# Kernel tuning notes

Measured on AMD Instinct MI355X. Metric: run time of the kernel, lower is better.

Reference implementation:

```python
import jax, jax.numpy as jnp
import numpy as np

B, S, HID, H, DH = 8, 4096, 1024, 16, 64


def setup_inputs() -> dict:
    key = jax.random.key(0)
    ks = jax.random.split(key, 5)
    return {
        "hidden_states": jax.random.normal(ks[0], (B, S, HID), dtype=jnp.float32),
        "attention_mask": jnp.ones((B, 1, 1, S), dtype=jnp.float32),
        "Wq": jax.random.normal(ks[1], (HID, HID), dtype=jnp.float32) * (HID ** -0.5),
        "Wk": jax.random.normal(ks[2], (HID, HID), dtype=jnp.float32) * (HID ** -0.5),
        "Wv": jax.random.normal(ks[3], (HID, HID), dtype=jnp.float32) * (HID ** -0.5),
        "att_weight": jax.random.normal(ks[4], (H, 1, DH), dtype=jnp.float32) * (DH ** -0.5),
    }


def _heads(x):
    # [B,S,HID] -> [B,H,S,DH]
    b, s, _ = x.shape
    return x.reshape(b, s, H, DH).transpose(0, 2, 1, 3)


def reference(hidden_states, attention_mask, Wq, Wk, Wv, att_weight):
    # bias-free projections (torch Linear: x @ W.T)
    q = _heads(hidden_states @ Wq.T)  # [B,H,S,DH]
    k = _heads(hidden_states @ Wk.T)
    v = _heads(hidden_states @ Wv.T)

    mask = attention_mask.transpose(0, 1, 3, 2)  # [B,1,S,1]
    aw = att_weight[:, 0, :]  # [H,DH]

    q_scores = jnp.einsum('bhsd,hd->bhs', q, aw)[..., None] * mask  # [B,H,S,1]
    k_scores = jnp.einsum('bhsd,hd->bhs', k, aw)[..., None] * mask  # [B,H,S,1]

    length = jnp.sum(mask, axis=-2, keepdims=True)            # [B,1,1,1]
    mean_value = jnp.sum(v * mask, axis=-2, keepdims=True)    # [B,H,1,DH]

    query_values = q_scores * mean_value                      # [B,H,S,DH] outer product
    key_values = jnp.einsum('bhs,bhsd->bhd', k_scores[..., 0], v)[:, :, None, :]  # [B,H,1,DH]

    ctx = (query_values + key_values) / length                # [B,H,S,DH]
    ctx = ctx.transpose(0, 2, 1, 3).reshape(ctx.shape[0], ctx.shape[2], H * DH)
    return ctx
```

## Files before the change

### kernel.cpp

```cpp
#include <hip/hip_runtime.h>

#define BB 8
#define SS 4096
#define HIDD 1024
#define HH 16
#define DHH 64

__global__ __launch_bounds__(256) void k_prep(const float* __restrict__ Wq,
                                              const float* __restrict__ Wk,
                                              const float* __restrict__ aw,
                                              float* __restrict__ wq_f,
                                              float* __restrict__ wk_f) {
    int i = blockIdx.x * 256 + threadIdx.x;
    int h = blockIdx.y;
    const float* W = blockIdx.z ? Wk : Wq;
    float* outp = blockIdx.z ? wk_f : wq_f;
    float acc = 0.f;
#pragma unroll
    for (int d = 0; d < DHH; ++d) {
        acc += aw[h * DHH + d] * W[(size_t)(h * DHH + d) * HIDD + i];
    }
    outp[h * HIDD + i] = acc;
}

#define KC 64
#define NCH (HIDD / KC)
__global__ __launch_bounds__(512) void k_scores(const float* __restrict__ hid,
                                                const float* __restrict__ mask,
                                                const float* __restrict__ weff,
                                                float* __restrict__ qsb,
                                                float* __restrict__ ksb) {
    __shared__ float shh[2][128 * 17 * 4];
    __shared__ float shw[2][32 * 16 * 4];

    const int t    = threadIdx.x;
    const int lane = t & 63;
    const int wave = t >> 6;
    const int obase = __builtin_amdgcn_readfirstlane(wave * 4);

    const int row0 = blockIdx.x * 128 + lane;
    const int row1 = row0 + 64;
    const size_t gbase = (size_t)blockIdx.x * 128 * HIDD;

    int srow[5], scol[5];
#pragma unroll
    for (int j = 0; j < 5; ++j) {
        int f = (j < 4) ? (j * 512 + t) : (2048 + t);
        int r = f / 17;
        int c = f - r * 17;
        srow[j] = r;
        scol[j] = (c == 16) ? 0 : c;
    }
    const bool extra = (t < 128);

    auto stage = [&](int chunk, int buf) {
#pragma unroll
        for (int j = 0; j < 4; ++j) {
            const float* gp = hid + gbase + (size_t)srow[j] * HIDD
                              + chunk * KC + scol[j] * 4;
            float* lp = &shh[buf][(j * 512 + t) * 4];
            __builtin_amdgcn_global_load_lds(
                (const __attribute__((address_space(1))) void*)gp,
                (__attribute__((address_space(3))) void*)lp, 16, 0, 0);
        }
        if (extra) {
            const float* gp = hid + gbase + (size_t)srow[4] * HIDD
                              + chunk * KC + scol[4] * 4;
            float* lp = &shh[buf][(2048 + t) * 4];
            __builtin_amdgcn_global_load_lds(
                (const __attribute__((address_space(1))) void*)gp,
                (__attribute__((address_space(3))) void*)lp, 16, 0, 0);
        }
        {
            const float* gp = weff + (size_t)(t >> 4) * HIDD
                              + chunk * KC + (t & 15) * 4;
            float* lp = &shw[buf][t * 4];
            __builtin_amdgcn_global_load_lds(
                (const __attribute__((address_space(1))) void*)gp,
                (__attribute__((address_space(3))) void*)lp, 16, 0, 0);
        }
    };

    float acc0[4] = {0.f, 0.f, 0.f, 0.f};
    float acc1[4] = {0.f, 0.f, 0.f, 0.f};

    stage(0, 0);

    for (int chunk = 0; chunk < NCH; ++chunk) {
        const int buf = chunk & 1;
        asm volatile("s_waitcnt vmcnt(0)" ::: "memory");
        __syncthreads();
        if (chunk + 1 < NCH) stage(chunk + 1, buf ^ 1);

        const float* h0 = &shh[buf][lane * 68];
        const float* h1 = &shh[buf][(lane + 64) * 68];
        const float* wb = &shw[buf][obase * 64];
#pragma unroll
        for (int kc = 0; kc < 16; ++kc) {
            float4 a0 = *reinterpret_cast<const float4*>(h0 + kc * 4);
            float4 a1 = *reinterpret_cast<const float4*>(h1 + kc * 4);
#pragma unroll
            for (int o = 0; o < 4; ++o) {
                float4 wv = *reinterpret_cast<const float4*>(wb + o * 64 + kc * 4);
                acc0[o] += a0.x * wv.x + a0.y * wv.y + a0.z * wv.z + a0.w * wv.w;
                acc1[o] += a1.x * wv.x + a1.y * wv.y + a1.z * wv.z + a1.w * wv.w;
            }
        }
    }

    float m0 = mask[row0];
    float m1 = mask[row1];
#pragma unroll
    for (int o = 0; o < 4; ++o) { acc0[o] *= m0; acc1[o] *= m1; }

    float4 v0 = make_float4(acc0[0], acc0[1], acc0[2], acc0[3]);
    float4 v1 = make_float4(acc1[0], acc1[1], acc1[2], acc1[3]);
    if (obase < 16) {
        *reinterpret_cast<float4*>(qsb + (size_t)row0 * 16 + obase) = v0;
        *reinterpret_cast<float4*>(qsb + (size_t)row1 * 16 + obase) = v1;
    } else {
        *reinterpret_cast<float4*>(ksb + (size_t)row0 * 20 + (obase - 16)) = v0;
        *reinterpret_cast<float4*>(ksb + (size_t)row1 * 20 + (obase - 16)) = v1;
        if (obase == 16) {
            ksb[(size_t)row0 * 20 + 16] = m0;
            ksb[(size_t)row1 * 20 + 16] = m1;
        }
    }
}

__global__ __launch_bounds__(256) void k_ksh(const float* __restrict__ hid,
                                             const float* __restrict__ ksb,
                                             float* __restrict__ part) {
    int b  = blockIdx.y;
    int i  = threadIdx.x * 4;
    int s0 = blockIdx.x * 64;

    float4 acc[17];
#pragma unroll
    for (int c = 0; c < 17; ++c) acc[c] = make_float4(0.f, 0.f, 0.f, 0.f);

    const float* hb = hid + (size_t)(b * SS + s0) * HIDD + i;
    const float* sb = ksb + (size_t)(b * SS + s0) * 20;

#pragma unroll 4
    for (int s = 0; s < 64; ++s) {
        float4 hv = *reinterpret_cast<const float4*>(hb + (size_t)s * HIDD);
        const float* sc = sb + s * 20;
#pragma unroll
        for (int c = 0; c < 17; ++c) {
            float scv = sc[c];
            acc[c].x += scv * hv.x;
            acc[c].y += scv * hv.y;
            acc[c].z += scv * hv.z;
            acc[c].w += scv * hv.w;
        }
    }

    float* pb = part + (((size_t)blockIdx.x * 8 + b) * 17) * 1024 + i;
#pragma unroll
    for (int c = 0; c < 17; ++c) {
        *reinterpret_cast<float4*>(pb + c * 1024) = acc[c];
    }
}

__global__ __launch_bounds__(256) void k_red(const float* __restrict__ part,
                                             float* __restrict__ ksh,
                                             float* __restrict__ hsum) {
    int gid = blockIdx.x * 256 + threadIdx.x;
    int b = gid / 17408;
    int r = gid - b * 17408;
    int c = r >> 10;
    int i = r & 1023;

    float s = 0.f;
#pragma unroll 8
    for (int k = 0; k < 64; ++k)
        s += part[(((size_t)k * 8 + b) * 17 + c) * 1024 + i];

    if (c < 16) ksh[((size_t)b * 16 + c) * 1024 + i] = s;
    else        hsum[b * 1024 + i] = s;
}

__global__ __launch_bounds__(256) void k_fin(const float* __restrict__ Wv,
                                             const float* __restrict__ mask,
                                             const float* __restrict__ hsum,
                                             const float* __restrict__ ksh,
                                             float* __restrict__ mvn,
                                             float* __restrict__ kvn) {
    int b  = blockIdx.x;
    int j  = blockIdx.y * 32 + (threadIdx.x >> 3);
    int sl = threadIdx.x & 7;

    __shared__ float red[256];
    float lsum = 0.f;
    for (int s = threadIdx.x; s < SS; s += 256) lsum += mask[b * SS + s];
    red[threadIdx.x] = lsum;
    __syncthreads();
    for (int off = 128; off; off >>= 1) {
        if (threadIdx.x < off) red[threadIdx.x] += red[threadIdx.x + off];
        __syncthreads();
    }
    float invlen = 1.0f / red[0];

    int h = j >> 6;
    const float4* w4 = reinterpret_cast<const float4*>(Wv + (size_t)j * HIDD + sl * 128);
    const float4* hv = reinterpret_cast<const float4*>(hsum + b * HIDD + sl * 128);
    const float4* kv = reinterpret_cast<const float4*>(ksh + ((size_t)b * 16 + h) * HIDD + sl * 128);

    float mv = 0.f, kvv = 0.f;
#pragma unroll
    for (int c = 0; c < 32; ++c) {
        float4 w = w4[c], a = hv[c], k2 = kv[c];
        mv  += w.x * a.x  + w.y * a.y  + w.z * a.z  + w.w * a.w;
        kvv += w.x * k2.x + w.y * k2.y + w.z * k2.z + w.w * k2.w;
    }
#pragma unroll
    for (int off = 1; off < 8; off <<= 1) {
        mv  += __shfl_xor(mv, off);
        kvv += __shfl_xor(kvv, off);
    }
    if (sl == 0) {
        mvn[b * HIDD + j] = mv * invlen;
        kvn[b * HIDD + j] = kvv * invlen;
    }
}

__global__ __launch_bounds__(256) void k_out(const float* __restrict__ qsb,
                                             const float* __restrict__ mvn,
                                             const float* __restrict__ kvn,
                                             float* __restrict__ outp) {
    size_t e0 = ((size_t)blockIdx.x * 256 + threadIdx.x) * 8;
    int b   = (int)(e0 >> 22);
    int rem = (int)(e0 & ((1u << 22) - 1));
    int s   = rem >> 10;
    int j   = rem & 1023;

    float q = qsb[(size_t)(b * SS + s) * 16 + (j >> 6)];
    const float4* mv4 = reinterpret_cast<const float4*>(mvn + b * HIDD + j);
    const float4* kv4 = reinterpret_cast<const float4*>(kvn + b * HIDD + j);
    float4 m0 = mv4[0], m1 = mv4[1];
    float4 k0 = kv4[0], k1 = kv4[1];

    float4 o0, o1;
    o0.x = q * m0.x + k0.x;  o0.y = q * m0.y + k0.y;
    o0.z = q * m0.z + k0.z;  o0.w = q * m0.w + k0.w;
    o1.x = q * m1.x + k1.x;  o1.y = q * m1.y + k1.y;
    o1.z = q * m1.z + k1.z;  o1.w = q * m1.w + k1.w;

    float4* op = reinterpret_cast<float4*>(outp + e0);
    op[0] = o0;
    op[1] = o1;
}

extern "C" void kernel_launch(void* const* d_in, const int* in_sizes, int n_in,
                              void* d_out, int out_size, void* d_ws, size_t ws_size,
                              hipStream_t stream) {
    const float* hid  = (const float*)d_in[0];
    const float* mask = (const float*)d_in[1];
    const float* Wq   = (const float*)d_in[2];
    const float* Wk   = (const float*)d_in[3];
    const float* Wv   = (const float*)d_in[4];
    const float* aw   = (const float*)d_in[5];
    float* outp = (float*)d_out;

    float* ws   = (float*)d_ws;
    float* wq_f = ws;
    float* wk_f = wq_f + 16384;
    float* qsb  = wk_f + 16384;
    float* ksb  = qsb + 524288;
    float* ksh  = ksb + 655360;
    float* hsum = ksh + 131072;
    float* mvn  = hsum + 8192;
    float* kvn  = mvn + 8192;
    float* part = kvn + 8192;

    k_prep  <<<dim3(4, 16, 2), 256, 0, stream>>>(Wq, Wk, aw, wq_f, wk_f);
    k_scores<<<dim3(256),      512, 0, stream>>>(hid, mask, wq_f, qsb, ksb);
    k_ksh   <<<dim3(64, 8),    256, 0, stream>>>(hid, ksb, part);
    k_red   <<<dim3(544),      256, 0, stream>>>(part, ksh, hsum);
    k_fin   <<<dim3(8, 32),    256, 0, stream>>>(Wv, mask, hsum, ksh, mvn, kvn);
    k_out   <<<dim3(16384),    256, 0, stream>>>(qsb, mvn, kvn, outp);
}
```

Before: 346.2 us.

## Compute score projections with split-bf16 MFMA instead of FP32 FMA

The k_scores GEMM (hidden x 32 effective weight columns) now runs on bf16 MFMA 16x16x32 instructions. Each fp32 value is split into hi+lo bf16 parts and three products are summed to stay close to fp32 accuracy. k_prep now writes the weights pre-split and pre-packed in the MFMA B-operand layout. The tile shrinks to 64 rows per 256-thread block with twice as many blocks. This cuts the FP32 ALU cost of the score GEMM, at the price of per-element conversion work on the A operand and some accuracy risk from the 3-term split.

```diff
diff --git a/kernel.cpp b/kernel.cpp
--- a/kernel.cpp
+++ b/kernel.cpp
@@ -6,59 +6,75 @@
 #define HH 16
 #define DHH 64
 
+typedef __attribute__((ext_vector_type(8))) short bf16x8;
+typedef __attribute__((ext_vector_type(4))) float f32x4;
+
+static __device__ __forceinline__ unsigned short f2bf(float x) {
+    union { float f; unsigned int u; } a; a.f = x;
+    unsigned int r = a.u + 0x7FFFu + ((a.u >> 16) & 1u);
+    return (unsigned short)(r >> 16);
+}
+static __device__ __forceinline__ float bf2f(unsigned short b) {
+    union { unsigned int u; float f; } a; a.u = ((unsigned int)b) << 16;
+    return a.f;
+}
+
 __global__ __launch_bounds__(256) void k_prep(const float* __restrict__ Wq,
                                               const float* __restrict__ Wk,
                                               const float* __restrict__ aw,
-                                              float* __restrict__ wq_f,
-                                              float* __restrict__ wk_f) {
-    int i = blockIdx.x * 256 + threadIdx.x;
+                                              unsigned short* __restrict__ bpack) {
+    int k = blockIdx.x * 256 + threadIdx.x;
     int h = blockIdx.y;
     const float* W = blockIdx.z ? Wk : Wq;
-    float* outp = blockIdx.z ? wk_f : wq_f;
+    int nt = blockIdx.z;
     float acc = 0.f;
 #pragma unroll
     for (int d = 0; d < DHH; ++d) {
-        acc += aw[h * DHH + d] * W[(size_t)(h * DHH + d) * HIDD + i];
-    }
-    outp[h * HIDD + i] = acc;
+        acc += aw[h * DHH + d] * W[(size_t)(h * DHH + d) * HIDD + k];
+    }
+    unsigned short hi = f2bf(acc);
+    unsigned short lo = f2bf(acc - bf2f(hi));
+    int kk   = k >> 5;
+    int r5   = (k >> 3) & 3;
+    int j    = k & 7;
+    int lane = r5 * 16 + h;
+    size_t baseh = ((size_t)(kk * 4 + 0 + nt) * 256 + lane * 4) * 2 + j;
+    size_t basel = ((size_t)(kk * 4 + 2 + nt) * 256 + lane * 4) * 2 + j;
+    bpack[baseh] = hi;
+    bpack[basel] = lo;
 }
 
 #define KC 64
-#define NCH (HIDD / KC)
-__global__ __launch_bounds__(512) void k_scores(const float* __restrict__ hid,
+__global__ __launch_bounds__(256) void k_scores(const float* __restrict__ hid,
                                                 const float* __restrict__ mask,
-                                                const float* __restrict__ weff,
+                                                const unsigned short* __restrict__ bpack,
                                                 float* __restrict__ qsb,
                                                 float* __restrict__ ksb) {
-    __shared__ float shh[2][128 * 17 * 4];
-    __shared__ float shw[2][32 * 16 * 4];
+    __shared__ float shh[2][64 * 68];
 
     const int t    = threadIdx.x;
     const int lane = t & 63;
     const int wave = t >> 6;
-    const int obase = __builtin_amdgcn_readfirstlane(wave * 4);
-
-    const int row0 = blockIdx.x * 128 + lane;
-    const int row1 = row0 + 64;
-    const size_t gbase = (size_t)blockIdx.x * 128 * HIDD;
+    const int rbase = blockIdx.x * 64;
+    const size_t gbase = (size_t)rbase * HIDD;
 
     int srow[5], scol[5];
 #pragma unroll
     for (int j = 0; j < 5; ++j) {
-        int f = (j < 4) ? (j * 512 + t) : (2048 + t);
+        int f = (j < 4) ? (j * 256 + t) : (1024 + t);
         int r = f / 17;
         int c = f - r * 17;
         srow[j] = r;
         scol[j] = (c == 16) ? 0 : c;
     }
-    const bool extra = (t < 128);
+    const bool extra = (t < 64);
 
     auto stage = [&](int chunk, int buf) {
 #pragma unroll
         for (int j = 0; j < 4; ++j) {
             const float* gp = hid + gbase + (size_t)srow[j] * HIDD
                               + chunk * KC + scol[j] * 4;
-            float* lp = &shh[buf][(j * 512 + t) * 4];
+            float* lp = &shh[buf][(j * 256 + t) * 4];
             __builtin_amdgcn_global_load_lds(
                 (const __attribute__((address_space(1))) void*)gp,
                 (__attribute__((address_space(3))) void*)lp, 16, 0, 0);
@@ -66,65 +82,64 @@
         if (extra) {
             const float* gp = hid + gbase + (size_t)srow[4] * HIDD
                               + chunk * KC + scol[4] * 4;
-            float* lp = &shh[buf][(2048 + t) * 4];
+            float* lp = &shh[buf][(1024 + t) * 4];
             __builtin_amdgcn_global_load_lds(
                 (const __attribute__((address_space(1))) void*)gp,
                 (__attribute__((address_space(3))) void*)lp, 16, 0, 0);
         }
-        {
-            const float* gp = weff + (size_t)(t >> 4) * HIDD
-                              + chunk * KC + (t & 15) * 4;
-            float* lp = &shw[buf][t * 4];
-            __builtin_amdgcn_global_load_lds(
-                (const __attribute__((address_space(1))) void*)gp,
-                (__attribute__((address_space(3))) void*)lp, 16, 0, 0);
-        }
     };
 
-    float acc0[4] = {0.f, 0.f, 0.f, 0.f};
-    float acc1[4] = {0.f, 0.f, 0.f, 0.f};
+    const bf16x8* bview = reinterpret_cast<const bf16x8*>(bpack);
+    const int mrow = wave * 16 + (lane & 15);
+    const int koff = (lane >> 4) * 8;
+
+    f32x4 accq = {0.f, 0.f, 0.f, 0.f};
+    f32x4 acck = {0.f, 0.f, 0.f, 0.f};
 
     stage(0, 0);
 
-    for (int chunk = 0; chunk < NCH; ++chunk) {
+    for (int chunk = 0; chunk < HIDD / KC; ++chunk) {
         const int buf = chunk & 1;
         asm volatile("s_waitcnt vmcnt(0)" ::: "memory");
         __syncthreads();
-        if (chunk + 1 < NCH) stage(chunk + 1, buf ^ 1);
-
-        const float* h0 = &shh[buf][lane * 68];
-        const float* h1 = &shh[buf][(lane + 64) * 68];
-        const float* wb = &shw[buf][obase * 64];
-#pragma unroll
-        for (int kc = 0; kc < 16; ++kc) {
-            float4 a0 = *reinterpret_cast<const float4*>(h0 + kc * 4);
-            float4 a1 = *reinterpret_cast<const float4*>(h1 + kc * 4);
-#pragma unroll
-            for (int o = 0; o < 4; ++o) {
-                float4 wv = *reinterpret_cast<const float4*>(wb + o * 64 + kc * 4);
-                acc0[o] += a0.x * wv.x + a0.y * wv.y + a0.z * wv.z + a0.w * wv.w;
-                acc1[o] += a1.x * wv.x + a1.y * wv.y + a1.z * wv.z + a1.w * wv.w;
+        if (chunk + 1 < HIDD / KC) stage(chunk + 1, buf ^ 1);
+
+#pragma unroll
+        for (int kl = 0; kl < 2; ++kl) {
+            const int kk = chunk * 2 + kl;
+            bf16x8 bh0 = bview[(kk * 4 + 0) * 64 + lane];
+            bf16x8 bh1 = bview[(kk * 4 + 1) * 64 + lane];
+            bf16x8 bl0 = bview[(kk * 4 + 2) * 64 + lane];
+            bf16x8 bl1 = bview[(kk * 4 + 3) * 64 + lane];
+
+            const float* ap = &shh[buf][mrow * 68 + kl * 32 + koff];
+            float4 av0 = *reinterpret_cast<const float4*>(ap);
+            float4 av1 = *reinterpret_cast<const float4*>(ap + 4);
+            float a[8] = {av0.x, av0.y, av0.z, av0.w, av1.x, av1.y, av1.z, av1.w};
+            union { bf16x8 v; unsigned short u[8]; } Ahi, Alo;
+#pragma unroll
+            for (int j = 0; j < 8; ++j) {
+                unsigned short hb = f2bf(a[j]);
+                Ahi.u[j] = hb;
+                Alo.u[j] = f2bf(a[j] - bf2f(hb));
             }
-        }
-    }
-
-    float m0 = mask[row0];
-    float m1 = mask[row1];
-#pragma unroll
-    for (int o = 0; o < 4; ++o) { acc0[o] *= m0; acc1[o] *= m1; }
-
-    float4 v0 = make_float4(acc0[0], acc0[1], acc0[2], acc0[3]);
-    float4 v1 = make_float4(acc1[0], acc1[1], acc1[2], acc1[3]);
-    if (obase < 16) {
-        *reinterpret_cast<float4*>(qsb + (size_t)row0 * 16 + obase) = v0;
-        *reinterpret_cast<float4*>(qsb + (size_t)row1 * 16 + obase) = v1;
-    } else {
-        *reinterpret_cast<float4*>(ksb + (size_t)row0 * 20 + (obase - 16)) = v0;
-        *reinterpret_cast<float4*>(ksb + (size_t)row1 * 20 + (obase - 16)) = v1;
-        if (obase == 16) {
-            ksb[(size_t)row0 * 20 + 16] = m0;
-            ksb[(size_t)row1 * 20 + 16] = m1;
-        }
+
+            accq = __builtin_amdgcn_mfma_f32_16x16x32_bf16(Ahi.v, bh0, accq, 0, 0, 0);
+            accq = __builtin_amdgcn_mfma_f32_16x16x32_bf16(Alo.v, bh0, accq, 0, 0, 0);
+            accq = __builtin_amdgcn_mfma_f32_16x16x32_bf16(Ahi.v, bl0, accq, 0, 0, 0);
+            acck = __builtin_amdgcn_mfma_f32_16x16x32_bf16(Ahi.v, bh1, acck, 0, 0, 0);
+            acck = __builtin_amdgcn_mfma_f32_16x16x32_bf16(Alo.v, bh1, acck, 0, 0, 0);
+            acck = __builtin_amdgcn_mfma_f32_16x16x32_bf16(Ahi.v, bl1, acck, 0, 0, 0);
+        }
+    }
+
+#pragma unroll
+    for (int reg = 0; reg < 4; ++reg) {
+        int grow = rbase + wave * 16 + (lane >> 4) * 4 + reg;
+        float m = mask[grow];
+        qsb[(size_t)grow * 16 + (lane & 15)] = accq[reg] * m;
+        ksb[(size_t)grow * 20 + (lane & 15)] = acck[reg] * m;
+        if ((lane & 15) == 0) ksb[(size_t)grow * 20 + 16] = m;
     }
 }
 
@@ -264,9 +279,8 @@
     float* outp = (float*)d_out;
 
     float* ws   = (float*)d_ws;
-    float* wq_f = ws;
-    float* wk_f = wq_f + 16384;
-    float* qsb  = wk_f + 16384;
+    unsigned short* bpack = (unsigned short*)ws;
+    float* qsb  = ws + 32768;
     float* ksb  = qsb + 524288;
     float* ksh  = ksb + 655360;
     float* hsum = ksh + 131072;
@@ -274,8 +288,8 @@
     float* kvn  = mvn + 8192;
     float* part = kvn + 8192;
 
-    k_prep  <<<dim3(4, 16, 2), 256, 0, stream>>>(Wq, Wk, aw, wq_f, wk_f);
-    k_scores<<<dim3(256),      512, 0, stream>>>(hid, mask, wq_f, qsb, ksb);
+    k_prep  <<<dim3(4, 16, 2), 256, 0, stream>>>(Wq, Wk, aw, bpack);
+    k_scores<<<dim3(512),      256, 0, stream>>>(hid, mask, bpack, qsb, ksb);
     k_ksh   <<<dim3(64, 8),    256, 0, stream>>>(hid, ksb, part);
     k_red   <<<dim3(544),      256, 0, stream>>>(part, ksh, hsum);
     k_fin   <<<dim3(8, 32),    256, 0, stream>>>(Wv, mask, hsum, ksh, mvn, kvn);
```

Measured after the change: 349.6 us. Within noise of the previous version (+1.0%).
